# Optimization experiments

Hardware: AMD Instinct MI355X
Metric: run time of the kernel (lower is better)

## Reference

```python
import jax, jax.numpy as jnp
import numpy as np

P, K, C = 16, 256, 3          # patches, boxes per patch, classes
PATCH = 1024                   # patch size (px)
SIZE_FACTOR = 1.0
IOU_T = 0.55                   # wbf_iou_thresh
PRE = P * K                    # pre_wbf_detections = 4096
POST = 1000                    # max_detections


def setup_inputs() -> dict:
    key = jax.random.key(0)
    k1, k2, k3, k4, k5, k6 = jax.random.split(key, 6)
    # realistic xyxy boxes inside a 1024px patch, 8..56 px wide
    cx = jax.random.uniform(k1, (P, K)) * (PATCH - 64)
    cy = jax.random.uniform(k2, (P, K)) * (PATCH - 64)
    w = jax.random.uniform(k3, (P, K)) * 48.0 + 8.0
    h = jax.random.uniform(k4, (P, K)) * 48.0 + 8.0
    b4 = jnp.stack([cx, cy, cx + w, cy + h], axis=-1)          # [P,K,4]
    scores = jax.random.uniform(k5, (P, K, 1))                  # (0,1)
    labels = jax.random.randint(k6, (P, K, 1), 0, C).astype(jnp.float32)
    boxes = jnp.concatenate([b4, scores, labels], axis=-1)      # [P,K,6]
    stride = float(int(PATCH * 0.8))
    grid = jnp.arange(4, dtype=jnp.float32) * stride
    ox = jnp.tile(grid, 4)
    oy = jnp.repeat(grid, 4)
    offsets = jnp.stack([ox, oy], axis=-1)                      # [P,2] (xmin,ymin)
    return {"boxes": boxes, "offsets": offsets}


def _wbf(dets):
    """Greedy class-aware weighted boxes fusion.

    dets: [N,6] = (x1,y1,x2,y2,score,label). Sequential scan: each box joins
    the first existing cluster of the SAME class with IoU(merged_box)>IOU_T,
    else opens a new cluster. Class-aware matching inside one scan is
    math-equivalent to the original per-class loops (clusters never mix
    classes; within-class order is preserved; output is score-sorted anyway).
    """
    N = dets.shape[0]
    init = (
        jnp.zeros((N, 4), jnp.float32),   # mbox: current merged box per slot
        jnp.zeros((N, 4), jnp.float32),   # wsum: sum(score*box)
        jnp.zeros((N,), jnp.float32),     # ssum: sum(score)
        jnp.zeros((N,), jnp.float32),     # cnt:  members per cluster
        jnp.full((N,), -1.0, jnp.float32),# cls:  cluster class id
        jnp.array(0, jnp.int32),          # num:  clusters opened so far
    )

    def step(carry, row):
        mbox, wsum, ssum, cnt, cls, num = carry
        box, score, label = row[:4], row[4], row[5]
        # IoU of `box` against every cluster slot (vectorized)
        xx1 = jnp.maximum(mbox[:, 0], box[0])
        yy1 = jnp.maximum(mbox[:, 1], box[1])
        xx2 = jnp.minimum(mbox[:, 2], box[2])
        yy2 = jnp.minimum(mbox[:, 3], box[3])
        inter = jnp.clip(xx2 - xx1, 0.0) * jnp.clip(yy2 - yy1, 0.0)
        area_a = (box[2] - box[0]) * (box[3] - box[1])
        area_b = (mbox[:, 2] - mbox[:, 0]) * (mbox[:, 3] - mbox[:, 1])
        union = area_a + area_b - inter
        iou = jnp.where(union > 0.0, inter / union, 0.0)
        match = (cnt > 0) & (cls == label) & (iou > IOU_T)
        has = jnp.any(match)
        idx = jnp.where(has, jnp.argmax(match).astype(jnp.int32), num)
        wsum = wsum.at[idx].add(score * box)
        ssum = ssum.at[idx].add(score)
        cnt = cnt.at[idx].add(1.0)
        mbox = mbox.at[idx].set(wsum[idx] / ssum[idx])
        cls = cls.at[idx].set(label)
        num = num + jnp.where(has, 0, 1).astype(jnp.int32)
        return (mbox, wsum, ssum, cnt, cls, num), None

    (mbox, wsum, ssum, cnt, cls, num), _ = jax.lax.scan(step, init, dets)
    valid = cnt > 0.0
    scores = jnp.where(valid, ssum / jnp.maximum(cnt, 1.0), 0.0)  # mean score
    return mbox, scores, cls, valid


def reference(boxes, offsets):
    # PatchMerger: shift boxes into global coords, rescale by size_factor
    off4 = jnp.concatenate([offsets, offsets], axis=-1)[:, None, :]  # [P,1,4]
    b4 = (boxes[..., :4] + off4) / SIZE_FACTOR                       # [P,K,4]
    dets = jnp.concatenate([b4, boxes[..., 4:]], axis=-1).reshape(-1, 6)[:PRE]
    # WBF clustering
    mbox, scores, cls, valid = _wbf(dets)
    # sort by score desc, keep top POST; pad rows zeroed
    sort_key = jnp.where(valid, scores, -1.0)
    topv, topi = jax.lax.top_k(sort_key, POST)
    out = jnp.concatenate([mbox, scores[:, None], cls[:, None]], axis=-1)[topi]
    out = jnp.where((topv >= 0.0)[:, None], out, 0.0)
    return out  # [POST, 6]
```

## Files before the change

### kernel.cpp

```cpp
#include <hip/hip_runtime.h>

#define N 4096
#define NT 1024
#define BATCH 64
#define KCAND 8
#define IOU_THR 0.55f
#define INF 0x7fffffff
#define NBINS 14
#define NBKT 42
#define BCAP 320

__device__ float4 g_wsum[N];

__device__ __forceinline__ float rl_f(float v, int lane) {
  return __int_as_float(__builtin_amdgcn_readlane(__float_as_int(v), lane));
}
__device__ __forceinline__ int rl_i(int v, int lane) {
  return __builtin_amdgcn_readlane(v, lane);
}

__global__ __launch_bounds__(NT) void wbf_kernel(
    const float* __restrict__ boxes,
    const float* __restrict__ offs,
    float* __restrict__ out)
{
  __shared__ float4 s_mbox[N];
  __shared__ float  s_ssum[N];
  __shared__ unsigned short s_cc[N];
  __shared__ unsigned short s_bkt[NBKT][BCAP];
  __shared__ int s_bktlen[NBKT];
  __shared__ unsigned long long s_dirty[64];
  __shared__ uint4 s_cand4[BATCH];
  __shared__ int   s_ccnt[BATCH];
  __shared__ float s_batch[BATCH][6];
  __shared__ unsigned s_bgate[BATCH];
  __shared__ unsigned long long s_pm[BATCH];
  __shared__ int s_min[2];
  __shared__ int s_num, s_resume, s_ovf;

  const int tid = threadIdx.x;

  if (tid < 64) s_dirty[tid] = 0ull;
  if (tid < NBKT) s_bktlen[tid] = 0;
  if (tid == 0) { s_num = 0; s_resume = BATCH; s_ovf = 0; s_min[0] = INF; s_min[1] = INF; }

  for (int t0 = 0; t0 < N; t0 += BATCH) {
    if (tid < BATCH * 6) {
      int b = tid / 6, f = tid % 6;
      int gi = t0 + b;
      float v = boxes[(size_t)gi * 6 + f];
      if (f < 4) v += offs[((gi >> 8) << 1) + (f & 1)];
      s_batch[b][f] = v;
    } else if (tid < BATCH * 7) {
      s_ccnt[tid - BATCH * 6] = 0;
    } else if (tid < BATCH * 8) {
      s_pm[tid - BATCH * 7] = 0ull;
    }
    __syncthreads();

    int nm0 = s_num;
    if (tid < BATCH) {
      int qx = (int)s_batch[tid][0];
      int qy = (int)s_batch[tid][1];
      int lb = (int)s_batch[tid][5];
      s_bgate[tid] = ((unsigned)((lb << 12) | qx) << 16) | (unsigned)qy;
    }
    __syncthreads();

    int use_linear = s_ovf;
    if (!use_linear) {
      int b = tid >> 4, sl = tid & 15;
      float qx1 = s_batch[b][0], qy1 = s_batch[b][1];
      float qx2 = s_batch[b][2], qy2 = s_batch[b][3];
      int cls = (int)s_batch[b][5];
      float aA = (qx2 - qx1) * (qy2 - qy1);
      int bb = ((int)qx1) >> 8;
      int jlo = bb > 0 ? bb - 1 : 0;
      int jhi = bb < NBINS - 1 ? bb + 1 : NBINS - 1;
      for (int j = jlo; j <= jhi; ++j) {
        int bk = cls * NBINS + j;
        int len = s_bktlen[bk]; if (len > BCAP) len = BCAP;
        for (int e = sl; e < len; e += 16) {
          int c = (int)s_bkt[bk][e];
          float4 m = s_mbox[c];
          if (fabsf(m.x - qx1) < 60.0f && fabsf(m.y - qy1) < 60.0f) {
            float xx1 = fmaxf(m.x, qx1), yy1 = fmaxf(m.y, qy1);
            float xx2 = fminf(m.z, qx2), yy2 = fminf(m.w, qy2);
            float iw = fmaxf(xx2 - xx1, 0.0f), ih = fmaxf(yy2 - yy1, 0.0f);
            float inter = iw * ih;
            float aB = (m.z - m.x) * (m.w - m.y);
            float uni = aA + aB - inter;
            if (uni > 0.0f && inter / uni > IOU_THR) {
              int pos = atomicAdd(&s_ccnt[b], 1);
              if (pos < KCAND) ((unsigned short*)&s_cand4[b])[pos] = (unsigned short)c;
            }
          }
        }
      }
    } else {
      for (int c = tid; c < nm0; c += NT) {
        float4 m = s_mbox[c];
        int mcls = (int)(s_cc[c] >> 14);
        float aB = (m.z - m.x) * (m.w - m.y);
        for (int b2 = 0; b2 < BATCH; ++b2) {
          float qx1 = s_batch[b2][0], qy1 = s_batch[b2][1];
          if (fabsf(m.x - qx1) < 60.0f && fabsf(m.y - qy1) < 60.0f &&
              mcls == (int)s_batch[b2][5]) {
            float qx2 = s_batch[b2][2], qy2 = s_batch[b2][3];
            float xx1 = fmaxf(m.x, qx1), yy1 = fmaxf(m.y, qy1);
            float xx2 = fminf(m.z, qx2), yy2 = fminf(m.w, qy2);
            float iw = fmaxf(xx2 - xx1, 0.0f), ih = fmaxf(yy2 - yy1, 0.0f);
            float inter = iw * ih;
            float aA = (qx2 - qx1) * (qy2 - qy1);
            float uni = aA + aB - inter;
            if (uni > 0.0f && inter / uni > IOU_THR) {
              int pos = atomicAdd(&s_ccnt[b2], 1);
              if (pos < KCAND) ((unsigned short*)&s_cand4[b2])[pos] = (unsigned short)c;
            }
          }
        }
      }
    }
    #pragma unroll
    for (int q = 0; q < 4; ++q) {
      int p = tid + q * NT;
      int bb2 = p >> 6, jj = p & 63;
      if (jj < bb2) {
        unsigned gb = s_bgate[bb2], gj = s_bgate[jj];
        unsigned dx = __usad(gb >> 16, gj >> 16, 0u);
        unsigned dy = __usad(gb & 0xFFFFu, gj & 0xFFFFu, 0u);
        if (dx <= 60u && dy <= 60u) {
          float ax1 = s_batch[bb2][0], ay1 = s_batch[bb2][1];
          float ax2 = s_batch[bb2][2], ay2 = s_batch[bb2][3];
          float jx1 = s_batch[jj][0], jy1 = s_batch[jj][1];
          float jx2 = s_batch[jj][2], jy2 = s_batch[jj][3];
          float xx1 = fmaxf(ax1, jx1), yy1 = fmaxf(ay1, jy1);
          float xx2 = fminf(ax2, jx2), yy2 = fminf(ay2, jy2);
          float iw = fmaxf(xx2 - xx1, 0.0f), ih = fmaxf(yy2 - yy1, 0.0f);
          float inter = iw * ih;
          float aA = (ax2 - ax1) * (ay2 - ay1);
          float aB = (jx2 - jx1) * (jy2 - jy1);
          float uni = aA + aB - inter;
          if (uni > 0.0f && inter / uni > IOU_THR)
            atomicOr(&s_pm[bb2], 1ull << jj);
        }
      }
    }
    __syncthreads();

    if (tid < 64) {
      const int lane = tid;
      float p0 = s_batch[lane][0], p1 = s_batch[lane][1], p2 = s_batch[lane][2];
      float p3 = s_batch[lane][3], p4 = s_batch[lane][4], p5 = s_batch[lane][5];
      int   cc_l = s_ccnt[lane];
      uint4 cp_l = s_cand4[lane];
      unsigned long long pm_l = s_pm[lane];
      int pml_lo = (int)(unsigned)pm_l, pml_hi = (int)(unsigned)(pm_l >> 32);
      int c0 = (int)(cp_l.x & 0xFFFFu);
      float4 wp0 = make_float4(0.f, 0.f, 0.f, 0.f);
      float ssp0 = 1.0f; int ctp0 = 0;
      if (cc_l > 0) { wp0 = g_wsum[c0]; ssp0 = s_ssum[c0]; ctp0 = (int)s_cc[c0]; }

      unsigned long long anycand = __ballot(cc_l > 0);
      unsigned long long OVF = __ballot(cc_l > KCAND);
      unsigned long long F = __ballot(cc_l > 0 || pm_l != 0ull);
      int rs = BATCH;
      if (OVF) rs = (int)__builtin_ctzll(OVF);
      unsigned long long lowrs = (rs >= 64) ? ~0ull : ((1ull << rs) - 1ull);
      unsigned long long rem = F & lowrs;
      unsigned long long NEWM = ~F & lowrs;
      unsigned long long consumed = 0ull;

      int nmod = 0;
      int e_valid = 0, e_idx = INF, e_ct = 0, e_origbb = -1;
      float e_cls = -1.0f;
      float e_m0=0,e_m1=0,e_m2=0,e_m3=0, e_w0=0,e_w1=0,e_w2=0,e_w3=0, e_ss=0;

      while (rem) {
        int b = (int)__builtin_ctzll(rem);
        rem &= rem - 1ull;
        float bx1 = rl_f(p0, b), by1 = rl_f(p1, b);
        float bx2 = rl_f(p2, b), by2 = rl_f(p3, b);
        float sc  = rl_f(p4, b), lbf = rl_f(p5, b);

        int v = INF;
        if (e_valid && e_cls == lbf &&
            fabsf(e_m0 - bx1) < 60.0f && fabsf(e_m1 - by1) < 60.0f) {
          float xx1 = fmaxf(e_m0, bx1), yy1 = fmaxf(e_m1, by1);
          float xx2 = fminf(e_m2, bx2), yy2 = fminf(e_m3, by2);
          float iw = fmaxf(xx2 - xx1, 0.0f), ih = fmaxf(yy2 - yy1, 0.0f);
          float inter = iw * ih;
          float aA = (bx2 - bx1) * (by2 - by1);
          float aB = (e_m2 - e_m0) * (e_m3 - e_m1);
          float uni = aA + aB - inter;
          if (uni > 0.0f && inter / uni > IOU_THR) v = e_idx;
        }
        if ((anycand >> b) & 1ull) {
          int cc = rl_i(cc_l, b);
          unsigned w0 = (unsigned)rl_i((int)cp_l.x, b);
          unsigned w1 = (unsigned)rl_i((int)cp_l.y, b);
          unsigned w2 = (unsigned)rl_i((int)cp_l.z, b);
          unsigned w3 = (unsigned)rl_i((int)cp_l.w, b);
          if (lane < cc) {
            unsigned w = (lane >= 6) ? w3 : (lane >= 4) ? w2 : (lane >= 2) ? w1 : w0;
            int ci = (int)((w >> ((lane & 1) * 16)) & 0xFFFFu);
            if (!((s_dirty[ci >> 6] >> (ci & 63)) & 1ull)) v = min(v, ci);
          }
        }
        unsigned long long ball = __ballot(v != INF);
        int mn = INF;
        if (ball != 0ull) {
          if (__popcll(ball) == 1) {
            mn = rl_i(v, (int)__builtin_ctzll(ball));
          } else {
            int t = v;
            for (int o = 32; o; o >>= 1) t = min(t, __shfl_xor(t, o));
            mn = t;
          }
        }
        unsigned long long pc =
            (((unsigned long long)(unsigned)rl_i(pml_hi, b)) << 32) |
            (unsigned long long)(unsigned)rl_i(pml_lo, b);
        pc &= ~F & ~consumed;
        int pj = 64, pairidx = INF;
        if (pc) {
          pj = (int)__builtin_ctzll(pc);
          pairidx = nm0 + (int)__builtin_popcountll(NEWM & ((1ull << pj) - 1ull));
        }
        if (pairidx < mn) mn = pairidx;

        if (mn == INF) {
          int nidx = nm0 + (int)__builtin_popcountll(NEWM & ((1ull << b) - 1ull));
          NEWM |= 1ull << b;
          if (lane == nmod) {
            e_valid = 1; e_idx = nidx; e_cls = lbf; e_origbb = -1;
            e_w0 = sc * bx1; e_w1 = sc * by1; e_w2 = sc * bx2; e_w3 = sc * by2;
            e_ss = sc; e_ct = 1;
            e_m0 = e_w0 / e_ss; e_m1 = e_w1 / e_ss; e_m2 = e_w2 / e_ss; e_m3 = e_w3 / e_ss;
          }
          nmod++;
        } else {
          bool mine = e_valid && (e_idx == mn);
          unsigned long long mb = __ballot(mine);
          int owner;
          if (mb != 0ull) {
            owner = (int)__builtin_ctzll(mb);
            if (mine) {
              e_w0 += sc * bx1; e_w1 += sc * by1; e_w2 += sc * bx2; e_w3 += sc * by2;
              e_ss += sc; e_ct += 1;
              e_m0 = e_w0 / e_ss; e_m1 = e_w1 / e_ss; e_m2 = e_w2 / e_ss; e_m3 = e_w3 / e_ss;
            }
          } else if (mn < nm0) {
            owner = nmod;
            int rc0 = rl_i(c0, b);
            if (lane == nmod) {
              float w0, w1, w2, w3, ss; int ctp;
              if (mn == rc0) {
                w0 = rl_f(wp0.x, b); w1 = rl_f(wp0.y, b);
                w2 = rl_f(wp0.z, b); w3 = rl_f(wp0.w, b);
                ss = rl_f(ssp0, b);  ctp = rl_i(ctp0, b);
              } else {
                float4 w = g_wsum[mn];
                w0 = w.x; w1 = w.y; w2 = w.z; w3 = w.w;
                ss = s_ssum[mn]; ctp = (int)s_cc[mn];
              }
              e_valid = 1; e_idx = mn; e_cls = lbf;
              e_origbb = ((int)(w0 / ss)) >> 8;
              e_w0 = w0 + sc * bx1; e_w1 = w1 + sc * by1;
              e_w2 = w2 + sc * bx2; e_w3 = w3 + sc * by2;
              e_ss = ss + sc; e_ct = (ctp & 0x3FFF) + 1;
              e_m0 = e_w0 / e_ss; e_m1 = e_w1 / e_ss; e_m2 = e_w2 / e_ss; e_m3 = e_w3 / e_ss;
              atomicOr(&s_dirty[mn >> 6], 1ull << (mn & 63));
            }
            nmod++;
          } else {
            owner = nmod;
            consumed |= 1ull << pj;
            if (lane == nmod) {
              float jx1 = rl_f(p0, pj), jy1 = rl_f(p1, pj);
              float jx2 = rl_f(p2, pj), jy2 = rl_f(p3, pj);
              float jsc = rl_f(p4, pj);
              e_valid = 1; e_idx = mn; e_cls = lbf; e_origbb = -1;
              e_w0 = jsc * jx1 + sc * bx1; e_w1 = jsc * jy1 + sc * by1;
              e_w2 = jsc * jx2 + sc * bx2; e_w3 = jsc * jy2 + sc * by2;
              e_ss = jsc + sc; e_ct = 2;
              e_m0 = e_w0 / e_ss; e_m1 = e_w1 / e_ss; e_m2 = e_w2 / e_ss; e_m3 = e_w3 / e_ss;
            }
            nmod++;
          }
          float nx1 = rl_f(e_m0, owner), ny1 = rl_f(e_m1, owner);
          float nx2 = rl_f(e_m2, owner), ny2 = rl_f(e_m3, owner);
          bool dp = false;
          if (p5 == lbf) {
            float xx1 = fmaxf(nx1, p0), yy1 = fmaxf(ny1, p1);
            float xx2 = fminf(nx2, p2), yy2 = fminf(ny2, p3);
            float iw = fmaxf(xx2 - xx1, 0.0f), ih = fmaxf(yy2 - yy1, 0.0f);
            float inter = iw * ih;
            float aA = (p2 - p0) * (p3 - p1);
            float aB = (nx2 - nx1) * (ny2 - ny1);
            float uni = aA + aB - inter;
            dp = (uni > 0.0f) && (inter / uni > IOU_THR);
          }
          unsigned long long det = __ballot(dp);
          unsigned long long himask = (b >= 63) ? 0ull : (~0ull << (b + 1));
          det &= ~F & ~consumed & lowrs & himask;
          if (det) { F |= det; rem |= det; NEWM &= ~det; }
        }
      }

      if (e_valid) {
        s_mbox[e_idx] = make_float4(e_m0, e_m1, e_m2, e_m3);
        g_wsum[e_idx] = make_float4(e_w0, e_w1, e_w2, e_w3);
        s_ssum[e_idx] = e_ss;
        s_cc[e_idx] = (unsigned short)(e_ct | (((int)e_cls) << 14));
        int nb = ((int)e_m0) >> 8;
        if (nb < 0) nb = 0; if (nb > NBINS - 1) nb = NBINS - 1;
        if (nb != e_origbb) {
          int bk = ((int)e_cls) * NBINS + nb;
          int p = atomicAdd(&s_bktlen[bk], 1);
          if (p < BCAP) s_bkt[bk][p] = (unsigned short)e_idx; else s_ovf = 1;
        }
      }
      {
        unsigned long long selfbit = 1ull << lane;
        if (NEWM & ~F & ~consumed & selfbit) {
          int idx = nm0 + (int)__builtin_popcountll(NEWM & (selfbit - 1ull));
          float w0 = p4 * p0, w1 = p4 * p1, w2 = p4 * p2, w3 = p4 * p3;
          float m0 = w0 / p4, m1 = w1 / p4, m2 = w2 / p4, m3 = w3 / p4;
          g_wsum[idx] = make_float4(w0, w1, w2, w3);
          s_ssum[idx] = p4;
          s_cc[idx] = (unsigned short)(1 | (((int)p5) << 14));
          s_mbox[idx] = make_float4(m0, m1, m2, m3);
          int nb = ((int)m0) >> 8;
          if (nb < 0) nb = 0; if (nb > NBINS - 1) nb = NBINS - 1;
          int bk = ((int)p5) * NBINS + nb;
          int p = atomicAdd(&s_bktlen[bk], 1);
          if (p < BCAP) s_bkt[bk][p] = (unsigned short)idx; else s_ovf = 1;
        }
      }
      s_dirty[lane] = 0ull;
      if (lane == 0) {
        s_num = nm0 + (int)__builtin_popcountll(NEWM);
        s_resume = rs;
      }
    }
    __syncthreads();

    int rs2 = s_resume;
    if (rs2 < BATCH) {
      for (int i = rs2; i < BATCH; ++i) {
        float bx1 = s_batch[i][0], by1 = s_batch[i][1];
        float bx2 = s_batch[i][2], by2 = s_batch[i][3];
        float sc  = s_batch[i][4];
        int lb = (int)s_batch[i][5];
        int nm = s_num;
        float aA = (bx2 - bx1) * (by2 - by1);
        int mymin = INF;
        for (int c = tid; c < nm; c += NT) {
          float4 m = s_mbox[c];
          if (fabsf(m.x - bx1) < 60.0f && fabsf(m.y - by1) < 60.0f &&
              (int)(s_cc[c] >> 14) == lb) {
            float xx1 = fmaxf(m.x, bx1), yy1 = fmaxf(m.y, by1);
            float xx2 = fminf(m.z, bx2), yy2 = fminf(m.w, by2);
            float iw = fmaxf(xx2 - xx1, 0.0f), ih = fmaxf(yy2 - yy1, 0.0f);
            float inter = iw * ih;
            float aB = (m.z - m.x) * (m.w - m.y);
            float uni = aA + aB - inter;
            if (uni > 0.0f && inter / uni > IOU_THR) mymin = min(mymin, c);
          }
        }
        if (mymin != INF) atomicMin(&s_min[i & 1], mymin);
        __syncthreads();
        int mn = s_min[i & 1];
        if (tid == 0) {
          s_min[(i + 1) & 1] = INF;
          bool has = (mn != INF);
          int idx = has ? mn : nm;
          float w0, w1, w2, w3, ss; int ct, ob = -1;
          if (has) {
            float4 w = g_wsum[idx];
            w0 = w.x; w1 = w.y; w2 = w.z; w3 = w.w;
            ss = s_ssum[idx]; ct = (int)(s_cc[idx] & 0x3FFF);
            ob = ((int)s_mbox[idx].x) >> 8;
          } else { w0 = w1 = w2 = w3 = 0.0f; ss = 0.0f; ct = 0; }
          w0 += sc * bx1; w1 += sc * by1; w2 += sc * bx2; w3 += sc * by2;
          ss += sc; ct += 1;
          float m0 = w0 / ss, m1 = w1 / ss, m2 = w2 / ss, m3 = w3 / ss;
          g_wsum[idx] = make_float4(w0, w1, w2, w3);
          s_ssum[idx] = ss;
          s_cc[idx] = (unsigned short)(ct | (lb << 14));
          s_mbox[idx] = make_float4(m0, m1, m2, m3);
          int nb = ((int)m0) >> 8;
          if (nb < 0) nb = 0; if (nb > NBINS - 1) nb = NBINS - 1;
          if (nb != ob) {
            int bk = lb * NBINS + nb;
            int p = atomicAdd(&s_bktlen[bk], 1);
            if (p < BCAP) s_bkt[bk][p] = (unsigned short)idx; else s_ovf = 1;
          }
          if (!has) s_num = nm + 1;
        }
        __syncthreads();
      }
      if (tid == 0) { s_min[0] = INF; s_min[1] = INF; }
    }
  }

  __syncthreads();
  unsigned long long* s_keys = (unsigned long long*)s_mbox;
  int num = s_num;
  for (int j = tid; j < N; j += NT) {
    unsigned int lo = ~(unsigned int)j;
    unsigned long long key;
    if (j < num) {
      float ct = (float)(s_cc[j] & 0x3FFF);
      float sco = s_ssum[j] / fmaxf(ct, 1.0f);
      unsigned int bb = __float_as_uint(sco) | 0x80000000u;
      key = ((unsigned long long)bb << 32) | lo;
    } else {
      key = (0x407FFFFFull << 32) | lo;
    }
    s_keys[j] = key;
  }
  __syncthreads();

  for (int k = 2; k <= N; k <<= 1) {
    for (int j = k >> 1; j > 0; j >>= 1) {
      #pragma unroll
      for (int w = 0; w < N / NT; ++w) {
        int a0 = tid + (w << 10);
        int l = a0 ^ j;
        if (l > a0) {
          unsigned long long a = s_keys[a0], bq = s_keys[l];
          bool desc = ((a0 & k) == 0);
          bool sw = desc ? (a < bq) : (a > bq);
          if (sw) { s_keys[a0] = bq; s_keys[l] = a; }
        }
      }
      __syncthreads();
    }
  }

  if (tid < 1000) {
    unsigned long long key = s_keys[tid];
    unsigned int hi = (unsigned int)(key >> 32);
    float* o = out + (size_t)tid * 6;
    if (hi & 0x80000000u) {
      int j = (int)(~(unsigned int)key);
      float4 w = g_wsum[j];
      float ss = s_ssum[j];
      o[0] = w.x / ss; o[1] = w.y / ss; o[2] = w.z / ss; o[3] = w.w / ss;
      o[4] = __uint_as_float(hi & 0x7FFFFFFFu);
      o[5] = (float)(s_cc[j] >> 14);
    } else {
      o[0] = 0.0f; o[1] = 0.0f; o[2] = 0.0f;
      o[3] = 0.0f; o[4] = 0.0f; o[5] = 0.0f;
    }
  }
}

extern "C" void kernel_launch(void* const* d_in, const int* in_sizes, int n_in,
                              void* d_out, int out_size, void* d_ws, size_t ws_size,
                              hipStream_t stream) {
  const float* boxes = (const float*)d_in[0];
  const float* offs  = (const float*)d_in[1];
  float* out = (float*)d_out;
  hipLaunchKernelGGL(wbf_kernel, dim3(1), dim3(NT), 0, stream, boxes, offs, out);
}
```

Before: 307.7 us.

## Add packed integer gate array, register-resident dirty bitmap, and merged batch load

Adds a packed 16-bit x/y integer gate per cluster so the bucket scan prefilters candidates with a 32-bit LDS load and SAD compare before fetching the full float4 box. It replaces the shared-memory dirty bitmap and its atomics with per-lane register words queried via ds_bpermute. It also folds the gate computation into a single per-box load step, removing one barrier per batch, and pads the batch rows so they can be read as vector loads. The integer gate truncates coordinates, so the prefilter can differ slightly from the float test, and the extra gate array uses more LDS.

Result: slower. 325.9 us (+5.9%).

```diff
diff --git a/kernel.cpp b/kernel.cpp
--- a/kernel.cpp
+++ b/kernel.cpp
@@ -27,12 +27,12 @@
   __shared__ float4 s_mbox[N];
   __shared__ float  s_ssum[N];
   __shared__ unsigned short s_cc[N];
+  __shared__ unsigned s_gate32[N];
   __shared__ unsigned short s_bkt[NBKT][BCAP];
   __shared__ int s_bktlen[NBKT];
-  __shared__ unsigned long long s_dirty[64];
   __shared__ uint4 s_cand4[BATCH];
   __shared__ int   s_ccnt[BATCH];
-  __shared__ float s_batch[BATCH][6];
+  __shared__ __align__(16) float s_batch[BATCH][8];
   __shared__ unsigned s_bgate[BATCH];
   __shared__ unsigned long long s_pm[BATCH];
   __shared__ int s_min[2];
@@ -40,39 +40,38 @@
 
   const int tid = threadIdx.x;
 
-  if (tid < 64) s_dirty[tid] = 0ull;
   if (tid < NBKT) s_bktlen[tid] = 0;
   if (tid == 0) { s_num = 0; s_resume = BATCH; s_ovf = 0; s_min[0] = INF; s_min[1] = INF; }
 
   for (int t0 = 0; t0 < N; t0 += BATCH) {
-    if (tid < BATCH * 6) {
-      int b = tid / 6, f = tid % 6;
-      int gi = t0 + b;
-      float v = boxes[(size_t)gi * 6 + f];
-      if (f < 4) v += offs[((gi >> 8) << 1) + (f & 1)];
-      s_batch[b][f] = v;
-    } else if (tid < BATCH * 7) {
-      s_ccnt[tid - BATCH * 6] = 0;
-    } else if (tid < BATCH * 8) {
-      s_pm[tid - BATCH * 7] = 0ull;
+    if (tid < BATCH) {
+      int gi = t0 + tid;
+      const float* br = boxes + (size_t)gi * 6;
+      int p = gi >> 8;
+      float ox = offs[2 * p], oy = offs[2 * p + 1];
+      float x1 = br[0] + ox, y1 = br[1] + oy;
+      float x2 = br[2] + ox, y2 = br[3] + oy;
+      float sc = br[4], lb = br[5];
+      s_batch[tid][0] = x1; s_batch[tid][1] = y1;
+      s_batch[tid][2] = x2; s_batch[tid][3] = y2;
+      s_batch[tid][4] = sc; s_batch[tid][5] = lb;
+      s_bgate[tid] = ((unsigned)(((int)lb << 12) | (int)x1) << 16) | (unsigned)(int)y1;
+    } else if (tid < 2 * BATCH) {
+      s_ccnt[tid - BATCH] = 0;
+    } else if (tid < 3 * BATCH) {
+      s_pm[tid - 2 * BATCH] = 0ull;
     }
     __syncthreads();
 
     int nm0 = s_num;
-    if (tid < BATCH) {
-      int qx = (int)s_batch[tid][0];
-      int qy = (int)s_batch[tid][1];
-      int lb = (int)s_batch[tid][5];
-      s_bgate[tid] = ((unsigned)((lb << 12) | qx) << 16) | (unsigned)qy;
-    }
-    __syncthreads();
-
     int use_linear = s_ovf;
+
     if (!use_linear) {
       int b = tid >> 4, sl = tid & 15;
       float qx1 = s_batch[b][0], qy1 = s_batch[b][1];
       float qx2 = s_batch[b][2], qy2 = s_batch[b][3];
       int cls = (int)s_batch[b][5];
+      unsigned qxq = (unsigned)(int)qx1, qyq = (unsigned)(int)qy1;
       float aA = (qx2 - qx1) * (qy2 - qy1);
       int bb = ((int)qx1) >> 8;
       int jlo = bb > 0 ? bb - 1 : 0;
@@ -82,8 +81,11 @@
         int len = s_bktlen[bk]; if (len > BCAP) len = BCAP;
         for (int e = sl; e < len; e += 16) {
           int c = (int)s_bkt[bk][e];
-          float4 m = s_mbox[c];
-          if (fabsf(m.x - qx1) < 60.0f && fabsf(m.y - qy1) < 60.0f) {
+          unsigned g = s_gate32[c];
+          unsigned dx = __usad(g >> 16, qxq, 0u);
+          unsigned dy = __usad(g & 0xFFFFu, qyq, 0u);
+          if (dx <= 60u && dy <= 60u) {
+            float4 m = s_mbox[c];
             float xx1 = fmaxf(m.x, qx1), yy1 = fmaxf(m.y, qy1);
             float xx2 = fminf(m.z, qx2), yy2 = fminf(m.w, qy2);
             float iw = fmaxf(xx2 - xx1, 0.0f), ih = fmaxf(yy2 - yy1, 0.0f);
@@ -150,8 +152,9 @@
 
     if (tid < 64) {
       const int lane = tid;
-      float p0 = s_batch[lane][0], p1 = s_batch[lane][1], p2 = s_batch[lane][2];
-      float p3 = s_batch[lane][3], p4 = s_batch[lane][4], p5 = s_batch[lane][5];
+      float4 qa = *(const float4*)&s_batch[lane][0];
+      float2 qb = *(const float2*)&s_batch[lane][4];
+      float p0 = qa.x, p1 = qa.y, p2 = qa.z, p3 = qa.w, p4 = qb.x, p5 = qb.y;
       int   cc_l = s_ccnt[lane];
       uint4 cp_l = s_cand4[lane];
       unsigned long long pm_l = s_pm[lane];
@@ -160,6 +163,8 @@
       float4 wp0 = make_float4(0.f, 0.f, 0.f, 0.f);
       float ssp0 = 1.0f; int ctp0 = 0;
       if (cc_l > 0) { wp0 = g_wsum[c0]; ssp0 = s_ssum[c0]; ctp0 = (int)s_cc[c0]; }
+
+      unsigned dlo = 0u, dhi = 0u;
 
       unsigned long long anycand = __ballot(cc_l > 0);
       unsigned long long OVF = __ballot(cc_l > KCAND);
@@ -201,11 +206,13 @@
           unsigned w1 = (unsigned)rl_i((int)cp_l.y, b);
           unsigned w2 = (unsigned)rl_i((int)cp_l.z, b);
           unsigned w3 = (unsigned)rl_i((int)cp_l.w, b);
-          if (lane < cc) {
-            unsigned w = (lane >= 6) ? w3 : (lane >= 4) ? w2 : (lane >= 2) ? w1 : w0;
-            int ci = (int)((w >> ((lane & 1) * 16)) & 0xFFFFu);
-            if (!((s_dirty[ci >> 6] >> (ci & 63)) & 1ull)) v = min(v, ci);
-          }
+          unsigned w = (lane >= 6) ? w3 : (lane >= 4) ? w2 : (lane >= 2) ? w1 : w0;
+          int ci = (int)((w >> ((lane & 1) * 16)) & 0xFFFFu);
+          int widx = (ci >> 6) & 63;
+          unsigned dl = (unsigned)__builtin_amdgcn_ds_bpermute(widx << 2, (int)dlo);
+          unsigned dh = (unsigned)__builtin_amdgcn_ds_bpermute(widx << 2, (int)dhi);
+          unsigned word = (ci & 32) ? dh : dl;
+          if (lane < cc && !((word >> (ci & 31)) & 1u)) v = min(v, ci);
         }
         unsigned long long ball = __ballot(v != INF);
         int mn = INF;
@@ -270,7 +277,9 @@
               e_w2 = w2 + sc * bx2; e_w3 = w3 + sc * by2;
               e_ss = ss + sc; e_ct = (ctp & 0x3FFF) + 1;
               e_m0 = e_w0 / e_ss; e_m1 = e_w1 / e_ss; e_m2 = e_w2 / e_ss; e_m3 = e_w3 / e_ss;
-              atomicOr(&s_dirty[mn >> 6], 1ull << (mn & 63));
+            }
+            if (lane == ((mn >> 6) & 63)) {
+              if (mn & 32) dhi |= 1u << (mn & 31); else dlo |= 1u << (mn & 31);
             }
             nmod++;
           } else {
@@ -313,6 +322,7 @@
         g_wsum[e_idx] = make_float4(e_w0, e_w1, e_w2, e_w3);
         s_ssum[e_idx] = e_ss;
         s_cc[e_idx] = (unsigned short)(e_ct | (((int)e_cls) << 14));
+        s_gate32[e_idx] = ((unsigned)(int)e_m0 << 16) | (unsigned)(int)e_m1;
         int nb = ((int)e_m0) >> 8;
         if (nb < 0) nb = 0; if (nb > NBINS - 1) nb = NBINS - 1;
         if (nb != e_origbb) {
@@ -331,6 +341,7 @@
           s_ssum[idx] = p4;
           s_cc[idx] = (unsigned short)(1 | (((int)p5) << 14));
           s_mbox[idx] = make_float4(m0, m1, m2, m3);
+          s_gate32[idx] = ((unsigned)(int)m0 << 16) | (unsigned)(int)m1;
           int nb = ((int)m0) >> 8;
           if (nb < 0) nb = 0; if (nb > NBINS - 1) nb = NBINS - 1;
           int bk = ((int)p5) * NBINS + nb;
@@ -338,7 +349,6 @@
           if (p < BCAP) s_bkt[bk][p] = (unsigned short)idx; else s_ovf = 1;
         }
       }
-      s_dirty[lane] = 0ull;
       if (lane == 0) {
         s_num = nm0 + (int)__builtin_popcountll(NEWM);
         s_resume = rs;
@@ -390,6 +400,7 @@
           s_ssum[idx] = ss;
           s_cc[idx] = (unsigned short)(ct | (lb << 14));
           s_mbox[idx] = make_float4(m0, m1, m2, m3);
+          s_gate32[idx] = ((unsigned)(int)m0 << 16) | (unsigned)(int)m1;
           int nb = ((int)m0) >> 8;
           if (nb < 0) nb = 0; if (nb > NBINS - 1) nb = NBINS - 1;
           if (nb != ob) {
```

## Add parallel fast path for batches with disjoint candidate clusters

Applied to the files above, without the earlier changes.

Adds a collision bitmap so the kernel can detect when no two boxes in a batch match the same existing cluster, no intra-batch pairs exist and no candidate list overflowed. In that case each lane merges its box into its minimum candidate cluster in parallel. A ballot-based check then verifies that no updated cluster captures another batch box, and the code falls back to the serial per-box loop if it does. This is meant to avoid the sequential wave-level scan for most batches. In exchange it adds extra LDS atomics during the candidate search and a verification pass.

Result: no change. 305.9 us (median of 2 runs) (-0.6%).

```diff
diff --git a/kernel.cpp b/kernel.cpp
--- a/kernel.cpp
+++ b/kernel.cpp
@@ -35,8 +35,9 @@
   __shared__ float s_batch[BATCH][6];
   __shared__ unsigned s_bgate[BATCH];
   __shared__ unsigned long long s_pm[BATCH];
+  __shared__ unsigned s_cbm[128];
   __shared__ int s_min[2];
-  __shared__ int s_num, s_resume, s_ovf;
+  __shared__ int s_num, s_resume, s_ovf, s_coll;
 
   const int tid = threadIdx.x;
 
@@ -55,6 +56,10 @@
       s_ccnt[tid - BATCH * 6] = 0;
     } else if (tid < BATCH * 8) {
       s_pm[tid - BATCH * 7] = 0ull;
+    } else if (tid < BATCH * 8 + 128) {
+      s_cbm[tid - BATCH * 8] = 0u;
+    } else if (tid == BATCH * 8 + 128) {
+      s_coll = 0;
     }
     __syncthreads();
 
@@ -93,6 +98,8 @@
             if (uni > 0.0f && inter / uni > IOU_THR) {
               int pos = atomicAdd(&s_ccnt[b], 1);
               if (pos < KCAND) ((unsigned short*)&s_cand4[b])[pos] = (unsigned short)c;
+              unsigned bit = 1u << (c & 31);
+              if (atomicOr(&s_cbm[c >> 5], bit) & bit) s_coll = 1;
             }
           }
         }
@@ -116,6 +123,8 @@
             if (uni > 0.0f && inter / uni > IOU_THR) {
               int pos = atomicAdd(&s_ccnt[b2], 1);
               if (pos < KCAND) ((unsigned short*)&s_cand4[b2])[pos] = (unsigned short)c;
+              unsigned bit = 1u << (c & 31);
+              if (atomicOr(&s_cbm[c >> 5], bit) & bit) s_coll = 1;
             }
           }
         }
@@ -155,15 +164,11 @@
       int   cc_l = s_ccnt[lane];
       uint4 cp_l = s_cand4[lane];
       unsigned long long pm_l = s_pm[lane];
-      int pml_lo = (int)(unsigned)pm_l, pml_hi = (int)(unsigned)(pm_l >> 32);
-      int c0 = (int)(cp_l.x & 0xFFFFu);
-      float4 wp0 = make_float4(0.f, 0.f, 0.f, 0.f);
-      float ssp0 = 1.0f; int ctp0 = 0;
-      if (cc_l > 0) { wp0 = g_wsum[c0]; ssp0 = s_ssum[c0]; ctp0 = (int)s_cc[c0]; }
 
       unsigned long long anycand = __ballot(cc_l > 0);
       unsigned long long OVF = __ballot(cc_l > KCAND);
-      unsigned long long F = __ballot(cc_l > 0 || pm_l != 0ull);
+      unsigned long long PAIRS = __ballot(pm_l != 0ull);
+      unsigned long long F = anycand | PAIRS;
       int rs = BATCH;
       if (OVF) rs = (int)__builtin_ctzll(OVF);
       unsigned long long lowrs = (rs >= 64) ? ~0ull : ((1ull << rs) - 1ull);
@@ -171,127 +176,40 @@
       unsigned long long NEWM = ~F & lowrs;
       unsigned long long consumed = 0ull;
 
+      int coll = s_coll;
+      bool fast = (OVF == 0ull) && (PAIRS == 0ull) && (coll == 0);
+
       int nmod = 0;
       int e_valid = 0, e_idx = INF, e_ct = 0, e_origbb = -1;
       float e_cls = -1.0f;
       float e_m0=0,e_m1=0,e_m2=0,e_m3=0, e_w0=0,e_w1=0,e_w2=0,e_w3=0, e_ss=0;
 
-      while (rem) {
-        int b = (int)__builtin_ctzll(rem);
-        rem &= rem - 1ull;
-        float bx1 = rl_f(p0, b), by1 = rl_f(p1, b);
-        float bx2 = rl_f(p2, b), by2 = rl_f(p3, b);
-        float sc  = rl_f(p4, b), lbf = rl_f(p5, b);
-
-        int v = INF;
-        if (e_valid && e_cls == lbf &&
-            fabsf(e_m0 - bx1) < 60.0f && fabsf(e_m1 - by1) < 60.0f) {
-          float xx1 = fmaxf(e_m0, bx1), yy1 = fmaxf(e_m1, by1);
-          float xx2 = fminf(e_m2, bx2), yy2 = fminf(e_m3, by2);
-          float iw = fmaxf(xx2 - xx1, 0.0f), ih = fmaxf(yy2 - yy1, 0.0f);
-          float inter = iw * ih;
-          float aA = (bx2 - bx1) * (by2 - by1);
-          float aB = (e_m2 - e_m0) * (e_m3 - e_m1);
-          float uni = aA + aB - inter;
-          if (uni > 0.0f && inter / uni > IOU_THR) v = e_idx;
-        }
-        if ((anycand >> b) & 1ull) {
-          int cc = rl_i(cc_l, b);
-          unsigned w0 = (unsigned)rl_i((int)cp_l.x, b);
-          unsigned w1 = (unsigned)rl_i((int)cp_l.y, b);
-          unsigned w2 = (unsigned)rl_i((int)cp_l.z, b);
-          unsigned w3 = (unsigned)rl_i((int)cp_l.w, b);
-          if (lane < cc) {
-            unsigned w = (lane >= 6) ? w3 : (lane >= 4) ? w2 : (lane >= 2) ? w1 : w0;
-            int ci = (int)((w >> ((lane & 1) * 16)) & 0xFFFFu);
-            if (!((s_dirty[ci >> 6] >> (ci & 63)) & 1ull)) v = min(v, ci);
-          }
-        }
-        unsigned long long ball = __ballot(v != INF);
-        int mn = INF;
-        if (ball != 0ull) {
-          if (__popcll(ball) == 1) {
-            mn = rl_i(v, (int)__builtin_ctzll(ball));
-          } else {
-            int t = v;
-            for (int o = 32; o; o >>= 1) t = min(t, __shfl_xor(t, o));
-            mn = t;
-          }
-        }
-        unsigned long long pc =
-            (((unsigned long long)(unsigned)rl_i(pml_hi, b)) << 32) |
-            (unsigned long long)(unsigned)rl_i(pml_lo, b);
-        pc &= ~F & ~consumed;
-        int pj = 64, pairidx = INF;
-        if (pc) {
-          pj = (int)__builtin_ctzll(pc);
-          pairidx = nm0 + (int)__builtin_popcountll(NEWM & ((1ull << pj) - 1ull));
-        }
-        if (pairidx < mn) mn = pairidx;
-
-        if (mn == INF) {
-          int nidx = nm0 + (int)__builtin_popcountll(NEWM & ((1ull << b) - 1ull));
-          NEWM |= 1ull << b;
-          if (lane == nmod) {
-            e_valid = 1; e_idx = nidx; e_cls = lbf; e_origbb = -1;
-            e_w0 = sc * bx1; e_w1 = sc * by1; e_w2 = sc * bx2; e_w3 = sc * by2;
-            e_ss = sc; e_ct = 1;
-            e_m0 = e_w0 / e_ss; e_m1 = e_w1 / e_ss; e_m2 = e_w2 / e_ss; e_m3 = e_w3 / e_ss;
-          }
-          nmod++;
-        } else {
-          bool mine = e_valid && (e_idx == mn);
-          unsigned long long mb = __ballot(mine);
-          int owner;
-          if (mb != 0ull) {
-            owner = (int)__builtin_ctzll(mb);
-            if (mine) {
-              e_w0 += sc * bx1; e_w1 += sc * by1; e_w2 += sc * bx2; e_w3 += sc * by2;
-              e_ss += sc; e_ct += 1;
-              e_m0 = e_w0 / e_ss; e_m1 = e_w1 / e_ss; e_m2 = e_w2 / e_ss; e_m3 = e_w3 / e_ss;
-            }
-          } else if (mn < nm0) {
-            owner = nmod;
-            int rc0 = rl_i(c0, b);
-            if (lane == nmod) {
-              float w0, w1, w2, w3, ss; int ctp;
-              if (mn == rc0) {
-                w0 = rl_f(wp0.x, b); w1 = rl_f(wp0.y, b);
-                w2 = rl_f(wp0.z, b); w3 = rl_f(wp0.w, b);
-                ss = rl_f(ssp0, b);  ctp = rl_i(ctp0, b);
-              } else {
-                float4 w = g_wsum[mn];
-                w0 = w.x; w1 = w.y; w2 = w.z; w3 = w.w;
-                ss = s_ssum[mn]; ctp = (int)s_cc[mn];
-              }
-              e_valid = 1; e_idx = mn; e_cls = lbf;
-              e_origbb = ((int)(w0 / ss)) >> 8;
-              e_w0 = w0 + sc * bx1; e_w1 = w1 + sc * by1;
-              e_w2 = w2 + sc * bx2; e_w3 = w3 + sc * by2;
-              e_ss = ss + sc; e_ct = (ctp & 0x3FFF) + 1;
-              e_m0 = e_w0 / e_ss; e_m1 = e_w1 / e_ss; e_m2 = e_w2 / e_ss; e_m3 = e_w3 / e_ss;
-              atomicOr(&s_dirty[mn >> 6], 1ull << (mn & 63));
-            }
-            nmod++;
-          } else {
-            owner = nmod;
-            consumed |= 1ull << pj;
-            if (lane == nmod) {
-              float jx1 = rl_f(p0, pj), jy1 = rl_f(p1, pj);
-              float jx2 = rl_f(p2, pj), jy2 = rl_f(p3, pj);
-              float jsc = rl_f(p4, pj);
-              e_valid = 1; e_idx = mn; e_cls = lbf; e_origbb = -1;
-              e_w0 = jsc * jx1 + sc * bx1; e_w1 = jsc * jy1 + sc * by1;
-              e_w2 = jsc * jx2 + sc * bx2; e_w3 = jsc * jy2 + sc * by2;
-              e_ss = jsc + sc; e_ct = 2;
-              e_m0 = e_w0 / e_ss; e_m1 = e_w1 / e_ss; e_m2 = e_w2 / e_ss; e_m3 = e_w3 / e_ss;
-            }
-            nmod++;
-          }
-          float nx1 = rl_f(e_m0, owner), ny1 = rl_f(e_m1, owner);
-          float nx2 = rl_f(e_m2, owner), ny2 = rl_f(e_m3, owner);
-          bool dp = false;
-          if (p5 == lbf) {
+      if (fast) {
+        bool merging = (cc_l > 0);
+        int mnl = INF;
+        const unsigned short* cl = (const unsigned short*)&cp_l;
+        #pragma unroll
+        for (int k = 0; k < KCAND; ++k)
+          if (k < cc_l) mnl = min(mnl, (int)cl[k]);
+        if (merging) {
+          float4 w = g_wsum[mnl];
+          float ss = s_ssum[mnl]; int ctp = (int)s_cc[mnl];
+          e_valid = 1; e_idx = mnl; e_cls = p5;
+          e_origbb = ((int)(w.x / ss)) >> 8;
+          e_w0 = w.x + p4 * p0; e_w1 = w.y + p4 * p1;
+          e_w2 = w.z + p4 * p2; e_w3 = w.w + p4 * p3;
+          e_ss = ss + p4; e_ct = (ctp & 0x3FFF) + 1;
+          e_m0 = e_w0 / e_ss; e_m1 = e_w1 / e_ss; e_m2 = e_w2 / e_ss; e_m3 = e_w3 / e_ss;
+        }
+        unsigned long long it = __ballot(merging);
+        bool bad = false;
+        while (it) {
+          int o = (int)__builtin_ctzll(it); it &= it - 1ull;
+          float nx1 = rl_f(e_m0, o), ny1 = rl_f(e_m1, o);
+          float nx2 = rl_f(e_m2, o), ny2 = rl_f(e_m3, o);
+          float ncls = rl_f(e_cls, o);
+          bool hit = false;
+          if (lane != o && p5 == ncls) {
             float xx1 = fmaxf(nx1, p0), yy1 = fmaxf(ny1, p1);
             float xx2 = fminf(nx2, p2), yy2 = fminf(ny2, p3);
             float iw = fmaxf(xx2 - xx1, 0.0f), ih = fmaxf(yy2 - yy1, 0.0f);
@@ -299,12 +217,154 @@
             float aA = (p2 - p0) * (p3 - p1);
             float aB = (nx2 - nx1) * (ny2 - ny1);
             float uni = aA + aB - inter;
-            dp = (uni > 0.0f) && (inter / uni > IOU_THR);
-          }
-          unsigned long long det = __ballot(dp);
-          unsigned long long himask = (b >= 63) ? 0ull : (~0ull << (b + 1));
-          det &= ~F & ~consumed & lowrs & himask;
-          if (det) { F |= det; rem |= det; NEWM &= ~det; }
+            hit = (uni > 0.0f) && (inter / uni > IOU_THR);
+          }
+          if (__ballot(hit) != 0ull) { bad = true; break; }
+        }
+        if (bad) {
+          fast = false;
+          e_valid = 0; e_idx = INF; e_ct = 0; e_origbb = -1; e_cls = -1.0f;
+          e_m0=e_m1=e_m2=e_m3=e_w0=e_w1=e_w2=e_w3=e_ss=0.0f;
+        }
+      }
+
+      if (!fast) {
+        int pml_lo = (int)(unsigned)pm_l, pml_hi = (int)(unsigned)(pm_l >> 32);
+        int c0 = (int)(cp_l.x & 0xFFFFu);
+        float4 wp0 = make_float4(0.f, 0.f, 0.f, 0.f);
+        float ssp0 = 1.0f; int ctp0 = 0;
+        if (cc_l > 0) { wp0 = g_wsum[c0]; ssp0 = s_ssum[c0]; ctp0 = (int)s_cc[c0]; }
+
+        while (rem) {
+          int b = (int)__builtin_ctzll(rem);
+          rem &= rem - 1ull;
+          float bx1 = rl_f(p0, b), by1 = rl_f(p1, b);
+          float bx2 = rl_f(p2, b), by2 = rl_f(p3, b);
+          float sc  = rl_f(p4, b), lbf = rl_f(p5, b);
+
+          int v = INF;
+          if (e_valid && e_cls == lbf &&
+              fabsf(e_m0 - bx1) < 60.0f && fabsf(e_m1 - by1) < 60.0f) {
+            float xx1 = fmaxf(e_m0, bx1), yy1 = fmaxf(e_m1, by1);
+            float xx2 = fminf(e_m2, bx2), yy2 = fminf(e_m3, by2);
+            float iw = fmaxf(xx2 - xx1, 0.0f), ih = fmaxf(yy2 - yy1, 0.0f);
+            float inter = iw * ih;
+            float aA = (bx2 - bx1) * (by2 - by1);
+            float aB = (e_m2 - e_m0) * (e_m3 - e_m1);
+            float uni = aA + aB - inter;
+            if (uni > 0.0f && inter / uni > IOU_THR) v = e_idx;
+          }
+          if ((anycand >> b) & 1ull) {
+            int cc = rl_i(cc_l, b);
+            unsigned w0 = (unsigned)rl_i((int)cp_l.x, b);
+            unsigned w1 = (unsigned)rl_i((int)cp_l.y, b);
+            unsigned w2 = (unsigned)rl_i((int)cp_l.z, b);
+            unsigned w3 = (unsigned)rl_i((int)cp_l.w, b);
+            if (lane < cc) {
+              unsigned w = (lane >= 6) ? w3 : (lane >= 4) ? w2 : (lane >= 2) ? w1 : w0;
+              int ci = (int)((w >> ((lane & 1) * 16)) & 0xFFFFu);
+              if (!((s_dirty[ci >> 6] >> (ci & 63)) & 1ull)) v = min(v, ci);
+            }
+          }
+          unsigned long long ball = __ballot(v != INF);
+          int mn = INF;
+          if (ball != 0ull) {
+            if (__popcll(ball) == 1) {
+              mn = rl_i(v, (int)__builtin_ctzll(ball));
+            } else {
+              int t = v;
+              for (int o = 32; o; o >>= 1) t = min(t, __shfl_xor(t, o));
+              mn = t;
+            }
+          }
+          unsigned long long pc =
+              (((unsigned long long)(unsigned)rl_i(pml_hi, b)) << 32) |
+              (unsigned long long)(unsigned)rl_i(pml_lo, b);
+          pc &= ~F & ~consumed;
+          int pj = 64, pairidx = INF;
+          if (pc) {
+            pj = (int)__builtin_ctzll(pc);
+            pairidx = nm0 + (int)__builtin_popcountll(NEWM & ((1ull << pj) - 1ull));
+          }
+          if (pairidx < mn) mn = pairidx;
+
+          if (mn == INF) {
+            int nidx = nm0 + (int)__builtin_popcountll(NEWM & ((1ull << b) - 1ull));
+            NEWM |= 1ull << b;
+            if (lane == nmod) {
+              e_valid = 1; e_idx = nidx; e_cls = lbf; e_origbb = -1;
+              e_w0 = sc * bx1; e_w1 = sc * by1; e_w2 = sc * bx2; e_w3 = sc * by2;
+              e_ss = sc; e_ct = 1;
+              e_m0 = e_w0 / e_ss; e_m1 = e_w1 / e_ss; e_m2 = e_w2 / e_ss; e_m3 = e_w3 / e_ss;
+            }
+            nmod++;
+          } else {
+            bool mine = e_valid && (e_idx == mn);
+            unsigned long long mb = __ballot(mine);
+            int owner;
+            if (mb != 0ull) {
+              owner = (int)__builtin_ctzll(mb);
+              if (mine) {
+                e_w0 += sc * bx1; e_w1 += sc * by1; e_w2 += sc * bx2; e_w3 += sc * by2;
+                e_ss += sc; e_ct += 1;
+                e_m0 = e_w0 / e_ss; e_m1 = e_w1 / e_ss; e_m2 = e_w2 / e_ss; e_m3 = e_w3 / e_ss;
+              }
+            } else if (mn < nm0) {
+              owner = nmod;
+              int rc0 = rl_i(c0, b);
+              if (lane == nmod) {
+                float w0, w1, w2, w3, ss; int ctp;
+                if (mn == rc0) {
+                  w0 = rl_f(wp0.x, b); w1 = rl_f(wp0.y, b);
+                  w2 = rl_f(wp0.z, b); w3 = rl_f(wp0.w, b);
+                  ss = rl_f(ssp0, b);  ctp = rl_i(ctp0, b);
+                } else {
+                  float4 w = g_wsum[mn];
+                  w0 = w.x; w1 = w.y; w2 = w.z; w3 = w.w;
+                  ss = s_ssum[mn]; ctp = (int)s_cc[mn];
+                }
+                e_valid = 1; e_idx = mn; e_cls = lbf;
+                e_origbb = ((int)(w0 / ss)) >> 8;
+                e_w0 = w0 + sc * bx1; e_w1 = w1 + sc * by1;
+                e_w2 = w2 + sc * bx2; e_w3 = w3 + sc * by2;
+                e_ss = ss + sc; e_ct = (ctp & 0x3FFF) + 1;
+                e_m0 = e_w0 / e_ss; e_m1 = e_w1 / e_ss; e_m2 = e_w2 / e_ss; e_m3 = e_w3 / e_ss;
+                atomicOr(&s_dirty[mn >> 6], 1ull << (mn & 63));
+              }
+              nmod++;
+            } else {
+              owner = nmod;
+              consumed |= 1ull << pj;
+              if (lane == nmod) {
+                float jx1 = rl_f(p0, pj), jy1 = rl_f(p1, pj);
+                float jx2 = rl_f(p2, pj), jy2 = rl_f(p3, pj);
+                float jsc = rl_f(p4, pj);
+                e_valid = 1; e_idx = mn; e_cls = lbf; e_origbb = -1;
+                e_w0 = jsc * jx1 + sc * bx1; e_w1 = jsc * jy1 + sc * by1;
+                e_w2 = jsc * jx2 + sc * bx2; e_w3 = jsc * jy2 + sc * by2;
+                e_ss = jsc + sc; e_ct = 2;
+                e_m0 = e_w0 / e_ss; e_m1 = e_w1 / e_ss; e_m2 = e_w2 / e_ss; e_m3 = e_w3 / e_ss;
+              }
+              nmod++;
+            }
+            float nx1 = rl_f(e_m0, owner), ny1 = rl_f(e_m1, owner);
+            float nx2 = rl_f(e_m2, owner), ny2 = rl_f(e_m3, owner);
+            bool dp = false;
+            if (p5 == rl_f(e_cls, owner)) {
+              float xx1 = fmaxf(nx1, p0), yy1 = fmaxf(ny1, p1);
+              float xx2 = fminf(nx2, p2), yy2 = fminf(ny2, p3);
+              float iw = fmaxf(xx2 - xx1, 0.0f), ih = fmaxf(yy2 - yy1, 0.0f);
+              float inter = iw * ih;
+              float aA = (p2 - p0) * (p3 - p1);
+              float aB = (nx2 - nx1) * (ny2 - ny1);
+              float uni = aA + aB - inter;
+              dp = (uni > 0.0f) && (inter / uni > IOU_THR);
+            }
+            unsigned long long det = __ballot(dp);
+            unsigned long long himask = (b >= 63) ? 0ull : (~0ull << (b + 1));
+            det &= ~F & ~consumed & lowrs & himask;
+            if (det) { F |= det; rem |= det; NEWM &= ~det; }
+          }
         }
       }
 
```

## Add packed integer gate array and restructure wave-serial merge with tagged min reduction

Applied to the files above, without the earlier changes.

Adds a packed 16-bit x/y integer gate per cluster so the bucket scan checks proximity with a 32-bit LDS load and sad instructions, and loads the full float4 box only for nearby clusters. The serial one-wave merge loop packs the cluster index with an owner tag into one value and finds the winner with a single shuffle-min reduction. This removes the ballot/owner search and unifies three update branches into one predicated update. The integer gate (truncation, <=60) is slightly looser than the float test, and it adds LDS writes at every cluster update.

Result: slower. 334.8 us (+8.8%).

```diff
diff --git a/kernel.cpp b/kernel.cpp
--- a/kernel.cpp
+++ b/kernel.cpp
@@ -27,6 +27,7 @@
   __shared__ float4 s_mbox[N];
   __shared__ float  s_ssum[N];
   __shared__ unsigned short s_cc[N];
+  __shared__ unsigned s_gate32[N];
   __shared__ unsigned short s_bkt[NBKT][BCAP];
   __shared__ int s_bktlen[NBKT];
   __shared__ unsigned long long s_dirty[64];
@@ -73,6 +74,7 @@
       float qx1 = s_batch[b][0], qy1 = s_batch[b][1];
       float qx2 = s_batch[b][2], qy2 = s_batch[b][3];
       int cls = (int)s_batch[b][5];
+      unsigned qxq = (unsigned)(int)qx1, qyq = (unsigned)(int)qy1;
       float aA = (qx2 - qx1) * (qy2 - qy1);
       int bb = ((int)qx1) >> 8;
       int jlo = bb > 0 ? bb - 1 : 0;
@@ -82,8 +84,11 @@
         int len = s_bktlen[bk]; if (len > BCAP) len = BCAP;
         for (int e = sl; e < len; e += 16) {
           int c = (int)s_bkt[bk][e];
-          float4 m = s_mbox[c];
-          if (fabsf(m.x - qx1) < 60.0f && fabsf(m.y - qy1) < 60.0f) {
+          unsigned g = s_gate32[c];
+          unsigned dx = __usad(g >> 16, qxq, 0u);
+          unsigned dy = __usad(g & 0xFFFFu, qyq, 0u);
+          if (dx <= 60u && dy <= 60u) {
+            float4 m = s_mbox[c];
             float xx1 = fmaxf(m.x, qx1), yy1 = fmaxf(m.y, qy1);
             float xx2 = fminf(m.z, qx2), yy2 = fminf(m.w, qy2);
             float iw = fmaxf(xx2 - xx1, 0.0f), ih = fmaxf(yy2 - yy1, 0.0f);
@@ -156,14 +161,21 @@
       uint4 cp_l = s_cand4[lane];
       unsigned long long pm_l = s_pm[lane];
       int pml_lo = (int)(unsigned)pm_l, pml_hi = (int)(unsigned)(pm_l >> 32);
-      int c0 = (int)(cp_l.x & 0xFFFFu);
+
+      const unsigned short* cl = (const unsigned short*)&cp_l;
+      int lim = cc_l < KCAND ? cc_l : KCAND;
+      int mnl = INF;
+      #pragma unroll
+      for (int k = 0; k < KCAND; ++k)
+        if (k < lim) mnl = min(mnl, (int)cl[k]);
       float4 wp0 = make_float4(0.f, 0.f, 0.f, 0.f);
       float ssp0 = 1.0f; int ctp0 = 0;
-      if (cc_l > 0) { wp0 = g_wsum[c0]; ssp0 = s_ssum[c0]; ctp0 = (int)s_cc[c0]; }
+      if (cc_l > 0) { wp0 = g_wsum[mnl]; ssp0 = s_ssum[mnl]; ctp0 = (int)s_cc[mnl]; }
 
       unsigned long long anycand = __ballot(cc_l > 0);
+      unsigned long long PAIRS = __ballot(pm_l != 0ull);
       unsigned long long OVF = __ballot(cc_l > KCAND);
-      unsigned long long F = __ballot(cc_l > 0 || pm_l != 0ull);
+      unsigned long long F = anycand | PAIRS;
       int rs = BATCH;
       if (OVF) rs = (int)__builtin_ctzll(OVF);
       unsigned long long lowrs = (rs >= 64) ? ~0ull : ((1ull << rs) - 1ull);
@@ -193,7 +205,7 @@
           float aA = (bx2 - bx1) * (by2 - by1);
           float aB = (e_m2 - e_m0) * (e_m3 - e_m1);
           float uni = aA + aB - inter;
-          if (uni > 0.0f && inter / uni > IOU_THR) v = e_idx;
+          if (uni > 0.0f && inter / uni > IOU_THR) v = (e_idx << 7) | lane;
         }
         if ((anycand >> b) & 1ull) {
           int cc = rl_i(cc_l, b);
@@ -204,58 +216,46 @@
           if (lane < cc) {
             unsigned w = (lane >= 6) ? w3 : (lane >= 4) ? w2 : (lane >= 2) ? w1 : w0;
             int ci = (int)((w >> ((lane & 1) * 16)) & 0xFFFFu);
-            if (!((s_dirty[ci >> 6] >> (ci & 63)) & 1ull)) v = min(v, ci);
-          }
-        }
-        unsigned long long ball = __ballot(v != INF);
-        int mn = INF;
-        if (ball != 0ull) {
-          if (__popcll(ball) == 1) {
-            mn = rl_i(v, (int)__builtin_ctzll(ball));
-          } else {
-            int t = v;
-            for (int o = 32; o; o >>= 1) t = min(t, __shfl_xor(t, o));
-            mn = t;
-          }
-        }
-        unsigned long long pc =
-            (((unsigned long long)(unsigned)rl_i(pml_hi, b)) << 32) |
-            (unsigned long long)(unsigned)rl_i(pml_lo, b);
-        pc &= ~F & ~consumed;
-        int pj = 64, pairidx = INF;
-        if (pc) {
-          pj = (int)__builtin_ctzll(pc);
-          pairidx = nm0 + (int)__builtin_popcountll(NEWM & ((1ull << pj) - 1ull));
-        }
-        if (pairidx < mn) mn = pairidx;
-
-        if (mn == INF) {
+            if (!((s_dirty[ci >> 6] >> (ci & 63)) & 1ull)) v = min(v, (ci << 7) | 64);
+          }
+        }
+        int t = v;
+        for (int o = 32; o; o >>= 1) t = min(t, __shfl_xor(t, o));
+        int pj = 64;
+        if ((PAIRS >> b) & 1ull) {
+          unsigned long long pc =
+              (((unsigned long long)(unsigned)rl_i(pml_hi, b)) << 32) |
+              (unsigned long long)(unsigned)rl_i(pml_lo, b);
+          pc &= ~F & ~consumed;
+          if (pc) {
+            pj = (int)__builtin_ctzll(pc);
+            int pairidx = nm0 + (int)__builtin_popcountll(NEWM & ((1ull << pj) - 1ull));
+            t = min(t, (pairidx << 7) | 127);
+          }
+        }
+
+        int take = 0, bidx = 0, bct = 0, borig = -1;
+        float bw0 = 0.f, bw1 = 0.f, bw2 = 0.f, bw3 = 0.f, bss = 0.f;
+        int owner = -1;
+        if (t == INF) {
           int nidx = nm0 + (int)__builtin_popcountll(NEWM & ((1ull << b) - 1ull));
           NEWM |= 1ull << b;
-          if (lane == nmod) {
-            e_valid = 1; e_idx = nidx; e_cls = lbf; e_origbb = -1;
-            e_w0 = sc * bx1; e_w1 = sc * by1; e_w2 = sc * bx2; e_w3 = sc * by2;
-            e_ss = sc; e_ct = 1;
-            e_m0 = e_w0 / e_ss; e_m1 = e_w1 / e_ss; e_m2 = e_w2 / e_ss; e_m3 = e_w3 / e_ss;
-          }
+          if (lane == nmod) { take = 1; bidx = nidx; }
           nmod++;
         } else {
-          bool mine = e_valid && (e_idx == mn);
-          unsigned long long mb = __ballot(mine);
-          int owner;
-          if (mb != 0ull) {
-            owner = (int)__builtin_ctzll(mb);
-            if (mine) {
-              e_w0 += sc * bx1; e_w1 += sc * by1; e_w2 += sc * bx2; e_w3 += sc * by2;
-              e_ss += sc; e_ct += 1;
-              e_m0 = e_w0 / e_ss; e_m1 = e_w1 / e_ss; e_m2 = e_w2 / e_ss; e_m3 = e_w3 / e_ss;
+          int mn = t >> 7, tag = t & 127;
+          if (tag < 64) {
+            owner = tag;
+            if (lane == tag) {
+              take = 1; bidx = e_idx; bct = e_ct; borig = e_origbb;
+              bw0 = e_w0; bw1 = e_w1; bw2 = e_w2; bw3 = e_w3; bss = e_ss;
             }
-          } else if (mn < nm0) {
+          } else if (tag == 64) {
             owner = nmod;
-            int rc0 = rl_i(c0, b);
+            int rmn = rl_i(mnl, b);
             if (lane == nmod) {
               float w0, w1, w2, w3, ss; int ctp;
-              if (mn == rc0) {
+              if (mn == rmn) {
                 w0 = rl_f(wp0.x, b); w1 = rl_f(wp0.y, b);
                 w2 = rl_f(wp0.z, b); w3 = rl_f(wp0.w, b);
                 ss = rl_f(ssp0, b);  ctp = rl_i(ctp0, b);
@@ -264,12 +264,9 @@
                 w0 = w.x; w1 = w.y; w2 = w.z; w3 = w.w;
                 ss = s_ssum[mn]; ctp = (int)s_cc[mn];
               }
-              e_valid = 1; e_idx = mn; e_cls = lbf;
-              e_origbb = ((int)(w0 / ss)) >> 8;
-              e_w0 = w0 + sc * bx1; e_w1 = w1 + sc * by1;
-              e_w2 = w2 + sc * bx2; e_w3 = w3 + sc * by2;
-              e_ss = ss + sc; e_ct = (ctp & 0x3FFF) + 1;
-              e_m0 = e_w0 / e_ss; e_m1 = e_w1 / e_ss; e_m2 = e_w2 / e_ss; e_m3 = e_w3 / e_ss;
+              take = 1; bidx = mn; bct = ctp & 0x3FFF;
+              borig = ((int)(w0 / ss)) >> 8;
+              bw0 = w0; bw1 = w1; bw2 = w2; bw3 = w3; bss = ss;
               atomicOr(&s_dirty[mn >> 6], 1ull << (mn & 63));
             }
             nmod++;
@@ -277,17 +274,24 @@
             owner = nmod;
             consumed |= 1ull << pj;
             if (lane == nmod) {
-              float jx1 = rl_f(p0, pj), jy1 = rl_f(p1, pj);
-              float jx2 = rl_f(p2, pj), jy2 = rl_f(p3, pj);
+              take = 1; bidx = mn; bct = 1;
               float jsc = rl_f(p4, pj);
-              e_valid = 1; e_idx = mn; e_cls = lbf; e_origbb = -1;
-              e_w0 = jsc * jx1 + sc * bx1; e_w1 = jsc * jy1 + sc * by1;
-              e_w2 = jsc * jx2 + sc * bx2; e_w3 = jsc * jy2 + sc * by2;
-              e_ss = jsc + sc; e_ct = 2;
-              e_m0 = e_w0 / e_ss; e_m1 = e_w1 / e_ss; e_m2 = e_w2 / e_ss; e_m3 = e_w3 / e_ss;
+              bw0 = jsc * rl_f(p0, pj); bw1 = jsc * rl_f(p1, pj);
+              bw2 = jsc * rl_f(p2, pj); bw3 = jsc * rl_f(p3, pj);
+              bss = jsc;
             }
             nmod++;
           }
+        }
+        if (take) {
+          e_valid = 1; e_idx = bidx; e_cls = lbf; e_origbb = borig; e_ct = bct + 1;
+          e_w0 = bw0 + sc * bx1; e_w1 = bw1 + sc * by1;
+          e_w2 = bw2 + sc * bx2; e_w3 = bw3 + sc * by2;
+          e_ss = bss + sc;
+          e_m0 = e_w0 / e_ss; e_m1 = e_w1 / e_ss;
+          e_m2 = e_w2 / e_ss; e_m3 = e_w3 / e_ss;
+        }
+        if (owner >= 0) {
           float nx1 = rl_f(e_m0, owner), ny1 = rl_f(e_m1, owner);
           float nx2 = rl_f(e_m2, owner), ny2 = rl_f(e_m3, owner);
           bool dp = false;
@@ -313,6 +317,7 @@
         g_wsum[e_idx] = make_float4(e_w0, e_w1, e_w2, e_w3);
         s_ssum[e_idx] = e_ss;
         s_cc[e_idx] = (unsigned short)(e_ct | (((int)e_cls) << 14));
+        s_gate32[e_idx] = ((unsigned)(int)e_m0 << 16) | (unsigned)(int)e_m1;
         int nb = ((int)e_m0) >> 8;
         if (nb < 0) nb = 0; if (nb > NBINS - 1) nb = NBINS - 1;
         if (nb != e_origbb) {
@@ -331,6 +336,7 @@
           s_ssum[idx] = p4;
           s_cc[idx] = (unsigned short)(1 | (((int)p5) << 14));
           s_mbox[idx] = make_float4(m0, m1, m2, m3);
+          s_gate32[idx] = ((unsigned)(int)m0 << 16) | (unsigned)(int)m1;
           int nb = ((int)m0) >> 8;
           if (nb < 0) nb = 0; if (nb > NBINS - 1) nb = NBINS - 1;
           int bk = ((int)p5) * NBINS + nb;
@@ -390,6 +396,7 @@
           s_ssum[idx] = ss;
           s_cc[idx] = (unsigned short)(ct | (lb << 14));
           s_mbox[idx] = make_float4(m0, m1, m2, m3);
+          s_gate32[idx] = ((unsigned)(int)m0 << 16) | (unsigned)(int)m1;
           int nb = ((int)m0) >> 8;
           if (nb < 0) nb = 0; if (nb > NBINS - 1) nb = NBINS - 1;
           if (nb != ob) {
```
